# Performance work log

Hardware: AMD Instinct MI355X
Metric: run time of the kernel (lower is better)

Reference implementation:

```python
import jax, jax.numpy as jnp
import numpy as np

WIN = (4, 8, 8)          # window_size (wd, wh, ww)
NUM_HEADS = 8
NW = 64                  # number of distinct shift-mask windows


def _relative_position_index(win):
    wd, wh, ww = win
    coords = np.stack(np.meshgrid(np.arange(wd), np.arange(wh), np.arange(ww), indexing='ij'))
    flat = coords.reshape(3, -1)                       # (3, N)
    rel = flat[:, :, None] - flat[:, None, :]          # (3, N, N)
    rel = rel.transpose(1, 2, 0).astype(np.int64)      # (N, N, 3)
    rel[..., 0] += wd - 1
    rel[..., 1] += wh - 1
    rel[..., 2] += ww - 1
    rel[..., 0] *= (2 * wh - 1) * (2 * ww - 1)
    rel[..., 1] *= (2 * ww - 1)
    return rel.sum(-1)                                 # (N, N)


def setup_inputs() -> dict:
    key = jax.random.key(0)
    ks = jax.random.split(key, 8)
    B_, C = 192, 256
    N = WIN[0] * WIN[1] * WIN[2]                       # 256 tokens per window
    table = (2 * WIN[0] - 1) * (2 * WIN[1] - 1) * (2 * WIN[2] - 1)  # 1575
    s = 0.02
    return {
        'x': jax.random.normal(ks[0], (B_, N, C), jnp.float32),
        'mask': jax.random.normal(ks[1], (NW, N, N), jnp.float32),
        'qkv_w': jax.random.normal(ks[2], (3 * C, C), jnp.float32) * s,
        'qkv_b': jax.random.normal(ks[3], (3 * C,), jnp.float32) * s,
        'proj_w': jax.random.normal(ks[4], (C, C), jnp.float32) * s,
        'proj_b': jax.random.normal(ks[5], (C,), jnp.float32) * s,
        'rel_pos_table': jax.random.normal(ks[6], (table, NUM_HEADS), jnp.float32) * s,
        'rel_pos_index': jnp.asarray(_relative_position_index(WIN), jnp.int32),
    }


def reference(x, mask, qkv_w, qkv_b, proj_w, proj_b, rel_pos_table, rel_pos_index):
    B_, N, C = x.shape
    H = NUM_HEADS
    hd = C // H
    scale = hd ** -0.5
    # qkv projection -> (3, B_, H, N, hd)
    qkv = (x @ qkv_w.T + qkv_b).reshape(B_, N, 3, H, hd).transpose(2, 0, 3, 1, 4)
    q, k, v = qkv[0], qkv[1], qkv[2]
    attn = jnp.einsum('bhnd,bhmd->bhnm', q * scale, k)            # (B_, H, N, N)
    # gathered relative-position bias: (N, N, H) -> (H, N, N)
    bias = rel_pos_table[rel_pos_index.reshape(-1)].reshape(N, N, H).transpose(2, 0, 1)
    attn = attn + bias[None]
    nW = mask.shape[0]
    attn = attn.reshape(B_ // nW, nW, H, N, N) + mask[None, :, None]
    attn = jax.nn.softmax(attn.reshape(B_, H, N, N), axis=-1)
    out = jnp.einsum('bhnm,bhmd->bhnd', attn, v)                  # (B_, H, N, hd)
    out = out.transpose(0, 2, 1, 3).reshape(B_, N, C)
    return out @ proj_w.T + proj_b
```

## Files before the change

kernel.cpp:

```cpp
#include <hip/hip_runtime.h>

typedef unsigned short ushort_t;
typedef __bf16 bf16x8 __attribute__((ext_vector_type(8)));
typedef float floatx4 __attribute__((ext_vector_type(4)));
typedef float floatx16 __attribute__((ext_vector_type(16)));

#define B_WIN 192
#define NTOK 256
#define CDIM 256
#define NHEAD 8
#define HDIM 32
#define NWIN 64
#define MROWS (B_WIN * NTOK)
#define LOG2E 1.4426950408889634f

__device__ __forceinline__ float bf2f(unsigned int b) {
  unsigned int u = (b & 0xffffu) << 16;
  float f; __builtin_memcpy(&f, &u, 4); return f;
}
__device__ __forceinline__ float uasf(unsigned int u) {
  float f; __builtin_memcpy(&f, &u, 4); return f;
}
__device__ __forceinline__ ushort_t f2bf(float f) {
  unsigned int u; __builtin_memcpy(&u, &f, 4);
  u = (u + 0x7fffu + ((u >> 16) & 1u)) >> 16;
  return (ushort_t)u;
}
__device__ __forceinline__ bf16x8 ldg8(const ushort_t* p) {
  return *reinterpret_cast<const bf16x8*>(p);
}
__device__ __forceinline__ void async_copy16(const void* g, void* l) {
  __builtin_amdgcn_global_load_lds(
      (const __attribute__((address_space(1))) unsigned int*)g,
      (__attribute__((address_space(3))) unsigned int*)l, 16, 0, 0);
}
__device__ __forceinline__ float fexp2(float x) {
  return __builtin_amdgcn_exp2f(x);
}
__device__ __forceinline__ unsigned pkbf(float a, float b) {
  return (unsigned)f2bf(a) | ((unsigned)f2bf(b) << 16);
}
__device__ __forceinline__ void plswap(unsigned& a, unsigned& b) {
  auto r = __builtin_amdgcn_permlane32_swap(a, b, false, false);
  a = r[0]; b = r[1];
}

__global__ __launch_bounds__(256) void cvt_f32_bf16(const float* __restrict__ src,
                                                    ushort_t* __restrict__ dst, int n8) {
  int t = blockIdx.x * 256 + threadIdx.x;
  if (t >= n8) return;
  const float4* s = reinterpret_cast<const float4*>(src) + (size_t)t * 2;
  float4 v0 = s[0], v1 = s[1];
  union { ushort_t u[8]; uint4 v; } pk;
  pk.u[0] = f2bf(v0.x); pk.u[1] = f2bf(v0.y); pk.u[2] = f2bf(v0.z); pk.u[3] = f2bf(v0.w);
  pk.u[4] = f2bf(v1.x); pk.u[5] = f2bf(v1.y); pk.u[6] = f2bf(v1.z); pk.u[7] = f2bf(v1.w);
  reinterpret_cast<uint4*>(dst)[t] = pk.v;
}

__global__ __launch_bounds__(256) void cvt_tile_w(const float* __restrict__ src,
                                                  ushort_t* __restrict__ dst, int n) {
  int t = blockIdx.x * 256 + threadIdx.x;
  if (t >= n) return;
  int col = t >> 5;
  int kk = (t & 31) * 8;
  const float4* s = reinterpret_cast<const float4*>(src + (size_t)col * 256 + kk);
  float4 v0 = s[0], v1 = s[1];
  union { ushort_t u[8]; uint4 v; } pk;
  pk.u[0] = f2bf(v0.x); pk.u[1] = f2bf(v0.y); pk.u[2] = f2bf(v0.z); pk.u[3] = f2bf(v0.w);
  pk.u[4] = f2bf(v1.x); pk.u[5] = f2bf(v1.y); pk.u[6] = f2bf(v1.z); pk.u[7] = f2bf(v1.w);
  size_t base = (size_t)(((col >> 4) * 8 + (kk >> 5)) * 512 + ((kk >> 3) & 3) * 128 + (col & 15) * 8);
  *reinterpret_cast<uint4*>(dst + base) = pk.v;
}

__global__ __launch_bounds__(256) void bm_prep(const int* __restrict__ idx,
                                               const float* __restrict__ table,
                                               const float* __restrict__ mask,
                                               ushort_t* __restrict__ bm) {
  const int win = blockIdx.x;
  const int qt = blockIdx.y;
  const int kb = blockIdx.z;
  const int l = threadIdx.x & 63;
  const int rg = threadIdx.x >> 6;
  const int tq = qt * 32 + (l & 31);
  const int hl = l >> 5;
  const int tk0 = kb * 32 + rg * 8 + hl * 4;

  const int4 ids = *reinterpret_cast<const int4*>(idx + tq * 256 + tk0);
  const float4 mv = *reinterpret_cast<const float4*>(mask + (size_t)win * 65536 + tq * 256 + tk0);
  const int idarr[4] = {ids.x, ids.y, ids.z, ids.w};
  const float marr[4] = {mv.x, mv.y, mv.z, mv.w};

  float v[8][4];
  #pragma unroll
  for (int r2 = 0; r2 < 4; ++r2) {
    const float* tr = table + (size_t)idarr[r2] * 8;
    float4 t0 = *reinterpret_cast<const float4*>(tr);
    float4 t1 = *reinterpret_cast<const float4*>(tr + 4);
    float m = marr[r2];
    v[0][r2] = (t0.x + m) * LOG2E; v[1][r2] = (t0.y + m) * LOG2E;
    v[2][r2] = (t0.z + m) * LOG2E; v[3][r2] = (t0.w + m) * LOG2E;
    v[4][r2] = (t1.x + m) * LOG2E; v[5][r2] = (t1.y + m) * LOG2E;
    v[6][r2] = (t1.z + m) * LOG2E; v[7][r2] = (t1.w + m) * LOG2E;
  }
  size_t base = ((size_t)((qt * 8 + kb) * 2 + (rg >> 1))) * 512 + l * 8 + (rg & 1) * 4;
  #pragma unroll
  for (int h = 0; h < 8; ++h) {
    union { ushort_t u[4]; uint2 w; } pk;
    pk.u[0] = f2bf(v[h][0]); pk.u[1] = f2bf(v[h][1]);
    pk.u[2] = f2bf(v[h][2]); pk.u[3] = f2bf(v[h][3]);
    *reinterpret_cast<uint2*>(bm + (((size_t)(win * 8 + h)) << 16) + base) = pk.w;
  }
}

__global__ __launch_bounds__(256) void qkv_gemm(
    const ushort_t* __restrict__ x, const ushort_t* __restrict__ wt,
    const float* __restrict__ qkvb, ushort_t* __restrict__ qws,
    ushort_t* __restrict__ kws, ushort_t* __restrict__ vtws) {
  const int lane = threadIdx.x & 63;
  const int wv = threadIdx.x >> 6;
  const int ln = lane & 15, qd = lane >> 4;
  const int row0 = blockIdx.x * 128 + (wv >> 1) * 64;
  const int col0 = blockIdx.y * 128;
  const int colw = col0 + (wv & 1) * 64;

  floatx4 acc[4][4];
  #pragma unroll
  for (int rt = 0; rt < 4; ++rt)
    #pragma unroll
    for (int ct = 0; ct < 4; ++ct)
      acc[rt][ct] = floatx4{0.f, 0.f, 0.f, 0.f};

  const ushort_t* ap = x + (size_t)(row0 + ln) * 256 + qd * 8;
  const ushort_t* bp = wt + (size_t)col0 * 256 + (wv & 1) * 16384 + qd * 128 + ln * 8;
  bf16x8 abuf[2][4], bbuf[2][4];
  #pragma unroll
  for (int t = 0; t < 4; ++t) {
    abuf[0][t] = ldg8(ap + t * 16 * 256);
    abuf[1][t] = ldg8(ap + t * 16 * 256 + 32);
    bbuf[0][t] = ldg8(bp + (t * 8 + 0) * 512);
    bbuf[1][t] = ldg8(bp + (t * 8 + 1) * 512);
  }

  #pragma unroll
  for (int kt = 0; kt < 8; ++kt) {
    #pragma unroll
    for (int rt = 0; rt < 4; ++rt)
      #pragma unroll
      for (int ct = 0; ct < 4; ++ct)
        acc[rt][ct] = __builtin_amdgcn_mfma_f32_16x16x32_bf16(abuf[kt & 1][rt], bbuf[kt & 1][ct],
                                                              acc[rt][ct], 0, 0, 0);
    if (kt < 6) {
      #pragma unroll
      for (int t = 0; t < 4; ++t) {
        abuf[kt & 1][t] = ldg8(ap + t * 16 * 256 + (kt + 2) * 32);
        bbuf[kt & 1][t] = ldg8(bp + (t * 8 + kt + 2) * 512);
      }
    }
  }

  const int s = colw >> 8;
  const float SCLQ = 0.17677669529663687f * LOG2E;
  #pragma unroll
  for (int ct = 0; ct < 4; ++ct) {
    int colg = colw + ct * 16 + ln;
    float bcol = qkvb[colg];
    int cs = colg & 255;
    int h = cs >> 5, d = cs & 31;
    int dslice = d >> 4, hh = (d >> 3) & 1, j = d & 7;
    #pragma unroll
    for (int rt = 0; rt < 4; ++rt) {
      int rbase = row0 + rt * 16 + qd * 4;
      int bwin = rbase >> 8, tok0 = rbase & 255;
      size_t slab = (size_t)(bwin * 8 + h) * 8192;
      if (s == 2) {
        int kt2 = tok0 >> 4, h2 = (tok0 >> 3) & 1, jj = tok0 & 7;
        union { ushort_t u[4]; uint2 v; } pk;
        #pragma unroll
        for (int i = 0; i < 4; ++i) pk.u[i] = f2bf(acc[rt][ct][i] + bcol);
        *reinterpret_cast<uint2*>(vtws + slab + kt2 * 512 + h2 * 256 + d * 8 + jj) = pk.v;
      } else {
        int blk = tok0 >> 5, c0 = tok0 & 31;
        size_t base = slab + (size_t)((blk * 2 + dslice) * 512 + hh * 256 + c0 * 8 + j);
        if (s == 0) {
          #pragma unroll
          for (int i = 0; i < 4; ++i)
            qws[base + i * 8] = f2bf((acc[rt][ct][i] + bcol) * SCLQ);
        } else {
          #pragma unroll
          for (int i = 0; i < 4; ++i)
            kws[base + i * 8] = f2bf(acc[rt][ct][i] + bcol);
        }
      }
    }
  }
}

__global__ __launch_bounds__(512, 4) void attn_kernel(
    const ushort_t* __restrict__ qws, const ushort_t* __restrict__ kws,
    const ushort_t* __restrict__ vtws, const ushort_t* __restrict__ bm,
    ushort_t* __restrict__ aows) {
  __shared__ __align__(16) ushort_t lds_kv[16384];
  __shared__ float inv_lds[256];
  const int lane = threadIdx.x & 63;
  const int wv = threadIdx.x >> 6;
  const int t = blockIdx.x;
  const int batch = t % 3;
  const int wh = t / 3;
  const int win = wh >> 3, h = wh & 7;
  const int bwin = batch * 64 + win;
  const int bh = bwin * 8 + h;

  {
    const char* kg = (const char*)(kws + (size_t)bh * 8192);
    const char* vg = (const char*)(vtws + (size_t)bh * 8192);
    #pragma unroll
    for (int r = 0; r < 2; ++r) {
      int off = r * 8192 + wv * 1024;
      async_copy16(kg + off + lane * 16, (char*)lds_kv + off);
      async_copy16(vg + off + lane * 16, (char*)lds_kv + 16384 + off);
    }
  }
  __syncthreads();

  const int qt = wv;
  const int hl = lane >> 5;
  const ushort_t* qb = qws + (size_t)bh * 8192 + qt * 1024 + lane * 8;
  const bf16x8 qf0 = ldg8(qb);
  const bf16x8 qf1 = ldg8(qb + 512);
  const ushort_t* bmp = bm + (((size_t)(win * 8 + h)) << 16) + qt * 8192 + lane * 8;

  floatx16 o;
  #pragma unroll
  for (int i = 0; i < 16; ++i) o[i] = 0.f;
  float ss0 = 0.f, ss1 = 0.f, ss2 = 0.f, ss3 = 0.f;

  #pragma unroll
  for (int kb = 0; kb < 8; ++kb) {
    const uint4 b0 = *reinterpret_cast<const uint4*>(bmp + kb * 1024);
    const uint4 b1 = *reinterpret_cast<const uint4*>(bmp + kb * 1024 + 512);
    floatx16 st;
    st[0]  = uasf(b0.x << 16); st[1]  = uasf(b0.x & 0xffff0000u);
    st[2]  = uasf(b0.y << 16); st[3]  = uasf(b0.y & 0xffff0000u);
    st[4]  = uasf(b0.z << 16); st[5]  = uasf(b0.z & 0xffff0000u);
    st[6]  = uasf(b0.w << 16); st[7]  = uasf(b0.w & 0xffff0000u);
    st[8]  = uasf(b1.x << 16); st[9]  = uasf(b1.x & 0xffff0000u);
    st[10] = uasf(b1.y << 16); st[11] = uasf(b1.y & 0xffff0000u);
    st[12] = uasf(b1.z << 16); st[13] = uasf(b1.z & 0xffff0000u);
    st[14] = uasf(b1.w << 16); st[15] = uasf(b1.w & 0xffff0000u);

    const bf16x8 kf0 = *reinterpret_cast<const bf16x8*>(&lds_kv[(kb * 2 + 0) * 512 + lane * 8]);
    const bf16x8 kf1 = *reinterpret_cast<const bf16x8*>(&lds_kv[(kb * 2 + 1) * 512 + lane * 8]);
    st = __builtin_amdgcn_mfma_f32_32x32x16_bf16(kf0, qf0, st, 0, 0, 0);
    st = __builtin_amdgcn_mfma_f32_32x32x16_bf16(kf1, qf1, st, 0, 0, 0);

    #pragma unroll
    for (int i = 0; i < 16; i += 4) {
      float e0 = fexp2(st[i]);     st[i]     = e0; ss0 += e0;
      float e1 = fexp2(st[i + 1]); st[i + 1] = e1; ss1 += e1;
      float e2 = fexp2(st[i + 2]); st[i + 2] = e2; ss2 += e2;
      float e3 = fexp2(st[i + 3]); st[i + 3] = e3; ss3 += e3;
    }

    unsigned p0 = pkbf(st[0], st[1]),   p1 = pkbf(st[2], st[3]);
    unsigned p2 = pkbf(st[4], st[5]),   p3 = pkbf(st[6], st[7]);
    unsigned p4 = pkbf(st[8], st[9]),   p5 = pkbf(st[10], st[11]);
    unsigned p6 = pkbf(st[12], st[13]), p7 = pkbf(st[14], st[15]);
    plswap(p0, p2);
    plswap(p1, p3);
    plswap(p4, p6);
    plswap(p5, p7);
    union { unsigned u[4]; bf16x8 v; } afe, afo;
    afe.u[0] = p0; afe.u[1] = p1; afe.u[2] = p2; afe.u[3] = p3;
    afo.u[0] = p4; afo.u[1] = p5; afo.u[2] = p6; afo.u[3] = p7;

    const bf16x8 bv0 = *reinterpret_cast<const bf16x8*>(&lds_kv[8192 + (kb * 2 + 0) * 512 + lane * 8]);
    const bf16x8 bv1 = *reinterpret_cast<const bf16x8*>(&lds_kv[8192 + (kb * 2 + 1) * 512 + lane * 8]);
    o = __builtin_amdgcn_mfma_f32_32x32x16_bf16(afe.v, bv0, o, 0, 0, 0);
    o = __builtin_amdgcn_mfma_f32_32x32x16_bf16(afo.v, bv1, o, 0, 0, 0);
  }

  float ssum = (ss0 + ss1) + (ss2 + ss3);
  ssum += __shfl_xor(ssum, 32, 64);
  const float inv = 1.0f / ssum;
  inv_lds[wv * 32 + (lane & 31)] = inv;
  __builtin_amdgcn_s_waitcnt(0);
  const float4 iv0 = *reinterpret_cast<const float4*>(&inv_lds[wv * 32 + 0 + hl * 4]);
  const float4 iv1 = *reinterpret_cast<const float4*>(&inv_lds[wv * 32 + 8 + hl * 4]);
  const float4 iv2 = *reinterpret_cast<const float4*>(&inv_lds[wv * 32 + 16 + hl * 4]);
  const float4 iv3 = *reinterpret_cast<const float4*>(&inv_lds[wv * 32 + 24 + hl * 4]);

  const int d = lane & 31;
  ushort_t* op = aows + (((size_t)bwin * 256 + qt * 32 + 4 * hl) << 8) + h * 32 + d;
  op[0 * 256]  = f2bf(o[0]  * iv0.x); op[1 * 256]  = f2bf(o[1]  * iv0.y);
  op[2 * 256]  = f2bf(o[2]  * iv0.z); op[3 * 256]  = f2bf(o[3]  * iv0.w);
  op[8 * 256]  = f2bf(o[4]  * iv1.x); op[9 * 256]  = f2bf(o[5]  * iv1.y);
  op[10 * 256] = f2bf(o[6]  * iv1.z); op[11 * 256] = f2bf(o[7]  * iv1.w);
  op[16 * 256] = f2bf(o[8]  * iv2.x); op[17 * 256] = f2bf(o[9]  * iv2.y);
  op[18 * 256] = f2bf(o[10] * iv2.z); op[19 * 256] = f2bf(o[11] * iv2.w);
  op[24 * 256] = f2bf(o[12] * iv3.x); op[25 * 256] = f2bf(o[13] * iv3.y);
  op[26 * 256] = f2bf(o[14] * iv3.z); op[27 * 256] = f2bf(o[15] * iv3.w);
}

__global__ __launch_bounds__(256) void proj_gemm(
    const ushort_t* __restrict__ a_, const ushort_t* __restrict__ wt,
    const float* __restrict__ pb, float* __restrict__ out) {
  const int lane = threadIdx.x & 63;
  const int wv = threadIdx.x >> 6;
  const int ln = lane & 15, qd = lane >> 4;
  const int row0 = blockIdx.x * 128 + (wv >> 1) * 64;
  const int col0 = blockIdx.y * 128;
  const int colw = col0 + (wv & 1) * 64;

  floatx4 acc[4][4];
  #pragma unroll
  for (int rt = 0; rt < 4; ++rt)
    #pragma unroll
    for (int ct = 0; ct < 4; ++ct)
      acc[rt][ct] = floatx4{0.f, 0.f, 0.f, 0.f};

  const ushort_t* ap = a_ + (size_t)(row0 + ln) * 256 + qd * 8;
  const ushort_t* bp = wt + (size_t)col0 * 256 + (wv & 1) * 16384 + qd * 128 + ln * 8;
  bf16x8 abuf[2][4], bbuf[2][4];
  #pragma unroll
  for (int t = 0; t < 4; ++t) {
    abuf[0][t] = ldg8(ap + t * 16 * 256);
    abuf[1][t] = ldg8(ap + t * 16 * 256 + 32);
    bbuf[0][t] = ldg8(bp + (t * 8 + 0) * 512);
    bbuf[1][t] = ldg8(bp + (t * 8 + 1) * 512);
  }

  #pragma unroll
  for (int kt = 0; kt < 8; ++kt) {
    #pragma unroll
    for (int rt = 0; rt < 4; ++rt)
      #pragma unroll
      for (int ct = 0; ct < 4; ++ct)
        acc[rt][ct] = __builtin_amdgcn_mfma_f32_16x16x32_bf16(abuf[kt & 1][rt], bbuf[kt & 1][ct],
                                                              acc[rt][ct], 0, 0, 0);
    if (kt < 6) {
      #pragma unroll
      for (int t = 0; t < 4; ++t) {
        abuf[kt & 1][t] = ldg8(ap + t * 16 * 256 + (kt + 2) * 32);
        bbuf[kt & 1][t] = ldg8(bp + (t * 8 + kt + 2) * 512);
      }
    }
  }

  #pragma unroll
  for (int ct = 0; ct < 4; ++ct) {
    int colg = colw + ct * 16 + ln;
    float bcol = pb[colg];
    #pragma unroll
    for (int rt = 0; rt < 4; ++rt) {
      int rbase = row0 + rt * 16 + qd * 4;
      #pragma unroll
      for (int i = 0; i < 4; ++i)
        out[(size_t)(rbase + i) * 256 + colg] = acc[rt][ct][i] + bcol;
    }
  }
}

extern "C" void kernel_launch(void* const* d_in, const int* in_sizes, int n_in,
                              void* d_out, int out_size, void* d_ws, size_t ws_size,
                              hipStream_t stream) {
  const float* x      = (const float*)d_in[0];
  const float* mask   = (const float*)d_in[1];
  const float* qkv_w  = (const float*)d_in[2];
  const float* qkv_b  = (const float*)d_in[3];
  const float* proj_w = (const float*)d_in[4];
  const float* proj_b = (const float*)d_in[5];
  const float* table  = (const float*)d_in[6];
  const int*   idx    = (const int*)d_in[7];
  float* out = (float*)d_out;

  char* ws = (char*)d_ws;
  const size_t SZ = (size_t)MROWS * CDIM * 2;
  ushort_t* xbf  = (ushort_t*)(ws);
  ushort_t* qws  = (ushort_t*)(ws + SZ);
  ushort_t* kws  = (ushort_t*)(ws + 2 * SZ);
  ushort_t* vtws = (ushort_t*)(ws + 3 * SZ);
  ushort_t* aows = (ushort_t*)(ws + 4 * SZ);
  ushort_t* bmws = (ushort_t*)(ws + 5 * SZ);
  ushort_t* wqkvbf  = (ushort_t*)(ws + 5 * SZ + 67108864);
  ushort_t* wprojbf = (ushort_t*)(ws + 5 * SZ + 67108864 + 393216);

  cvt_f32_bf16<<<dim3(6144), dim3(256), 0, stream>>>(x, xbf, 12582912 / 8);
  cvt_tile_w<<<dim3(96), dim3(256), 0, stream>>>(qkv_w, wqkvbf, 768 * 32);
  cvt_tile_w<<<dim3(32), dim3(256), 0, stream>>>(proj_w, wprojbf, 256 * 32);
  bm_prep<<<dim3(64, 8, 8), dim3(256), 0, stream>>>(idx, table, mask, bmws);
  qkv_gemm<<<dim3(384, 6), dim3(256), 0, stream>>>(xbf, wqkvbf, qkv_b, qws, kws, vtws);
  attn_kernel<<<dim3(1536), dim3(512), 0, stream>>>(qws, kws, vtws, bmws, aows);
  proj_gemm<<<dim3(384, 2), dim3(256), 0, stream>>>(aows, wprojbf, proj_b, out);
}
```

Measured before the change: 283.9 us.

## Split combined bias+mask into separate per-window mask and per-head bias buffers

Instead of precomputing a 64x8 window-by-head combined bias+mask tensor in bf16, this stores the mask per window and the relative-position bias per head, and adds them inside the attention kernel. That shrinks the prep output and the attention kernel's streamed footprint, and the small bias buffer stays cache-resident. In exchange, each score element needs an extra load and an add, and summing two rounded bf16 values adds a little error. The GEMM grids are also flattened with an XCD-aware block remap so that each XCD works on a contiguous range of row tiles, which should improve L2 reuse.

New measurement: 272.2 us. -4.1%, faster.

```diff
diff --git a/kernel.cpp b/kernel.cpp
--- a/kernel.cpp
+++ b/kernel.cpp
@@ -14,10 +14,6 @@
 #define MROWS (B_WIN * NTOK)
 #define LOG2E 1.4426950408889634f
 
-__device__ __forceinline__ float bf2f(unsigned int b) {
-  unsigned int u = (b & 0xffffu) << 16;
-  float f; __builtin_memcpy(&f, &u, 4); return f;
-}
 __device__ __forceinline__ float uasf(unsigned int u) {
   float f; __builtin_memcpy(&f, &u, 4); return f;
 }
@@ -72,10 +68,8 @@
   *reinterpret_cast<uint4*>(dst + base) = pk.v;
 }
 
-__global__ __launch_bounds__(256) void bm_prep(const int* __restrict__ idx,
-                                               const float* __restrict__ table,
-                                               const float* __restrict__ mask,
-                                               ushort_t* __restrict__ bm) {
+__global__ __launch_bounds__(256) void mask_prep(const float* __restrict__ mask,
+                                                 ushort_t* __restrict__ mf) {
   const int win = blockIdx.x;
   const int qt = blockIdx.y;
   const int kb = blockIdx.z;
@@ -84,23 +78,36 @@
   const int tq = qt * 32 + (l & 31);
   const int hl = l >> 5;
   const int tk0 = kb * 32 + rg * 8 + hl * 4;
-
+  const float4 mv = *reinterpret_cast<const float4*>(mask + (size_t)win * 65536 + tq * 256 + tk0);
+  union { ushort_t u[4]; uint2 w; } pk;
+  pk.u[0] = f2bf(mv.x * LOG2E); pk.u[1] = f2bf(mv.y * LOG2E);
+  pk.u[2] = f2bf(mv.z * LOG2E); pk.u[3] = f2bf(mv.w * LOG2E);
+  size_t base = ((size_t)((qt * 8 + kb) * 2 + (rg >> 1))) * 512 + l * 8 + (rg & 1) * 4;
+  *reinterpret_cast<uint2*>(mf + ((size_t)win << 16) + base) = pk.w;
+}
+
+__global__ __launch_bounds__(256) void bias_prep(const int* __restrict__ idx,
+                                                 const float* __restrict__ table,
+                                                 ushort_t* __restrict__ bf) {
+  const int qt = blockIdx.x;
+  const int kb = blockIdx.y;
+  const int l = threadIdx.x & 63;
+  const int rg = threadIdx.x >> 6;
+  const int tq = qt * 32 + (l & 31);
+  const int hl = l >> 5;
+  const int tk0 = kb * 32 + rg * 8 + hl * 4;
   const int4 ids = *reinterpret_cast<const int4*>(idx + tq * 256 + tk0);
-  const float4 mv = *reinterpret_cast<const float4*>(mask + (size_t)win * 65536 + tq * 256 + tk0);
   const int idarr[4] = {ids.x, ids.y, ids.z, ids.w};
-  const float marr[4] = {mv.x, mv.y, mv.z, mv.w};
-
   float v[8][4];
   #pragma unroll
   for (int r2 = 0; r2 < 4; ++r2) {
     const float* tr = table + (size_t)idarr[r2] * 8;
     float4 t0 = *reinterpret_cast<const float4*>(tr);
     float4 t1 = *reinterpret_cast<const float4*>(tr + 4);
-    float m = marr[r2];
-    v[0][r2] = (t0.x + m) * LOG2E; v[1][r2] = (t0.y + m) * LOG2E;
-    v[2][r2] = (t0.z + m) * LOG2E; v[3][r2] = (t0.w + m) * LOG2E;
-    v[4][r2] = (t1.x + m) * LOG2E; v[5][r2] = (t1.y + m) * LOG2E;
-    v[6][r2] = (t1.z + m) * LOG2E; v[7][r2] = (t1.w + m) * LOG2E;
+    v[0][r2] = t0.x * LOG2E; v[1][r2] = t0.y * LOG2E;
+    v[2][r2] = t0.z * LOG2E; v[3][r2] = t0.w * LOG2E;
+    v[4][r2] = t1.x * LOG2E; v[5][r2] = t1.y * LOG2E;
+    v[6][r2] = t1.z * LOG2E; v[7][r2] = t1.w * LOG2E;
   }
   size_t base = ((size_t)((qt * 8 + kb) * 2 + (rg >> 1))) * 512 + l * 8 + (rg & 1) * 4;
   #pragma unroll
@@ -108,7 +115,7 @@
     union { ushort_t u[4]; uint2 w; } pk;
     pk.u[0] = f2bf(v[h][0]); pk.u[1] = f2bf(v[h][1]);
     pk.u[2] = f2bf(v[h][2]); pk.u[3] = f2bf(v[h][3]);
-    *reinterpret_cast<uint2*>(bm + (((size_t)(win * 8 + h)) << 16) + base) = pk.w;
+    *reinterpret_cast<uint2*>(bf + ((size_t)h << 16) + base) = pk.w;
   }
 }
 
@@ -119,8 +126,12 @@
   const int lane = threadIdx.x & 63;
   const int wv = threadIdx.x >> 6;
   const int ln = lane & 15, qd = lane >> 4;
-  const int row0 = blockIdx.x * 128 + (wv >> 1) * 64;
-  const int col0 = blockIdx.y * 128;
+  const int b = blockIdx.x;
+  const int xcd = b & 7, lb = b >> 3;
+  const int rtile = xcd * 48 + (lb % 48);
+  const int ctile = lb / 48;
+  const int row0 = rtile * 128 + (wv >> 1) * 64;
+  const int col0 = ctile * 128;
   const int colw = col0 + (wv & 1) * 64;
 
   floatx4 acc[4][4];
@@ -197,8 +208,8 @@
 
 __global__ __launch_bounds__(512, 4) void attn_kernel(
     const ushort_t* __restrict__ qws, const ushort_t* __restrict__ kws,
-    const ushort_t* __restrict__ vtws, const ushort_t* __restrict__ bm,
-    ushort_t* __restrict__ aows) {
+    const ushort_t* __restrict__ vtws, const ushort_t* __restrict__ mf,
+    const ushort_t* __restrict__ bfr, ushort_t* __restrict__ aows) {
   __shared__ __align__(16) ushort_t lds_kv[16384];
   __shared__ float inv_lds[256];
   const int lane = threadIdx.x & 63;
@@ -227,7 +238,8 @@
   const ushort_t* qb = qws + (size_t)bh * 8192 + qt * 1024 + lane * 8;
   const bf16x8 qf0 = ldg8(qb);
   const bf16x8 qf1 = ldg8(qb + 512);
-  const ushort_t* bmp = bm + (((size_t)(win * 8 + h)) << 16) + qt * 8192 + lane * 8;
+  const ushort_t* mp = mf + ((size_t)win << 16) + qt * 8192 + lane * 8;
+  const ushort_t* cp = bfr + ((size_t)h << 16) + qt * 8192 + lane * 8;
 
   floatx16 o;
   #pragma unroll
@@ -236,17 +248,27 @@
 
   #pragma unroll
   for (int kb = 0; kb < 8; ++kb) {
-    const uint4 b0 = *reinterpret_cast<const uint4*>(bmp + kb * 1024);
-    const uint4 b1 = *reinterpret_cast<const uint4*>(bmp + kb * 1024 + 512);
+    const uint4 m0 = *reinterpret_cast<const uint4*>(mp + kb * 1024);
+    const uint4 m1 = *reinterpret_cast<const uint4*>(mp + kb * 1024 + 512);
+    const uint4 c0 = *reinterpret_cast<const uint4*>(cp + kb * 1024);
+    const uint4 c1 = *reinterpret_cast<const uint4*>(cp + kb * 1024 + 512);
     floatx16 st;
-    st[0]  = uasf(b0.x << 16); st[1]  = uasf(b0.x & 0xffff0000u);
-    st[2]  = uasf(b0.y << 16); st[3]  = uasf(b0.y & 0xffff0000u);
-    st[4]  = uasf(b0.z << 16); st[5]  = uasf(b0.z & 0xffff0000u);
-    st[6]  = uasf(b0.w << 16); st[7]  = uasf(b0.w & 0xffff0000u);
-    st[8]  = uasf(b1.x << 16); st[9]  = uasf(b1.x & 0xffff0000u);
-    st[10] = uasf(b1.y << 16); st[11] = uasf(b1.y & 0xffff0000u);
-    st[12] = uasf(b1.z << 16); st[13] = uasf(b1.z & 0xffff0000u);
-    st[14] = uasf(b1.w << 16); st[15] = uasf(b1.w & 0xffff0000u);
+    st[0]  = uasf(m0.x << 16) + uasf(c0.x << 16);
+    st[1]  = uasf(m0.x & 0xffff0000u) + uasf(c0.x & 0xffff0000u);
+    st[2]  = uasf(m0.y << 16) + uasf(c0.y << 16);
+    st[3]  = uasf(m0.y & 0xffff0000u) + uasf(c0.y & 0xffff0000u);
+    st[4]  = uasf(m0.z << 16) + uasf(c0.z << 16);
+    st[5]  = uasf(m0.z & 0xffff0000u) + uasf(c0.z & 0xffff0000u);
+    st[6]  = uasf(m0.w << 16) + uasf(c0.w << 16);
+    st[7]  = uasf(m0.w & 0xffff0000u) + uasf(c0.w & 0xffff0000u);
+    st[8]  = uasf(m1.x << 16) + uasf(c1.x << 16);
+    st[9]  = uasf(m1.x & 0xffff0000u) + uasf(c1.x & 0xffff0000u);
+    st[10] = uasf(m1.y << 16) + uasf(c1.y << 16);
+    st[11] = uasf(m1.y & 0xffff0000u) + uasf(c1.y & 0xffff0000u);
+    st[12] = uasf(m1.z << 16) + uasf(c1.z << 16);
+    st[13] = uasf(m1.z & 0xffff0000u) + uasf(c1.z & 0xffff0000u);
+    st[14] = uasf(m1.w << 16) + uasf(c1.w << 16);
+    st[15] = uasf(m1.w & 0xffff0000u) + uasf(c1.w & 0xffff0000u);
 
     const bf16x8 kf0 = *reinterpret_cast<const bf16x8*>(&lds_kv[(kb * 2 + 0) * 512 + lane * 8]);
     const bf16x8 kf1 = *reinterpret_cast<const bf16x8*>(&lds_kv[(kb * 2 + 1) * 512 + lane * 8]);
@@ -307,8 +329,12 @@
   const int lane = threadIdx.x & 63;
   const int wv = threadIdx.x >> 6;
   const int ln = lane & 15, qd = lane >> 4;
-  const int row0 = blockIdx.x * 128 + (wv >> 1) * 64;
-  const int col0 = blockIdx.y * 128;
+  const int b = blockIdx.x;
+  const int xcd = b & 7, lb = b >> 3;
+  const int rtile = xcd * 48 + (lb % 48);
+  const int ctile = lb / 48;
+  const int row0 = rtile * 128 + (wv >> 1) * 64;
+  const int col0 = ctile * 128;
   const int colw = col0 + (wv & 1) * 64;
 
   floatx4 acc[4][4];
@@ -380,15 +406,17 @@
   ushort_t* kws  = (ushort_t*)(ws + 2 * SZ);
   ushort_t* vtws = (ushort_t*)(ws + 3 * SZ);
   ushort_t* aows = (ushort_t*)(ws + 4 * SZ);
-  ushort_t* bmws = (ushort_t*)(ws + 5 * SZ);
-  ushort_t* wqkvbf  = (ushort_t*)(ws + 5 * SZ + 67108864);
-  ushort_t* wprojbf = (ushort_t*)(ws + 5 * SZ + 67108864 + 393216);
+  ushort_t* mfws = (ushort_t*)(ws + 5 * SZ);
+  ushort_t* bfws = (ushort_t*)(ws + 5 * SZ + 8388608);
+  ushort_t* wqkvbf  = (ushort_t*)(ws + 5 * SZ + 8388608 + 1048576);
+  ushort_t* wprojbf = (ushort_t*)(ws + 5 * SZ + 8388608 + 1048576 + 393216);
 
   cvt_f32_bf16<<<dim3(6144), dim3(256), 0, stream>>>(x, xbf, 12582912 / 8);
   cvt_tile_w<<<dim3(96), dim3(256), 0, stream>>>(qkv_w, wqkvbf, 768 * 32);
   cvt_tile_w<<<dim3(32), dim3(256), 0, stream>>>(proj_w, wprojbf, 256 * 32);
-  bm_prep<<<dim3(64, 8, 8), dim3(256), 0, stream>>>(idx, table, mask, bmws);
-  qkv_gemm<<<dim3(384, 6), dim3(256), 0, stream>>>(xbf, wqkvbf, qkv_b, qws, kws, vtws);
-  attn_kernel<<<dim3(1536), dim3(512), 0, stream>>>(qws, kws, vtws, bmws, aows);
-  proj_gemm<<<dim3(384, 2), dim3(256), 0, stream>>>(aows, wprojbf, proj_b, out);
-}
+  mask_prep<<<dim3(64, 8, 8), dim3(256), 0, stream>>>(mask, mfws);
+  bias_prep<<<dim3(8, 8), dim3(256), 0, stream>>>(idx, table, bfws);
+  qkv_gemm<<<dim3(2304), dim3(256), 0, stream>>>(xbf, wqkvbf, qkv_b, qws, kws, vtws);
+  attn_kernel<<<dim3(1536), dim3(512), 0, stream>>>(qws, kws, vtws, mfws, bfws, aows);
+  proj_gemm<<<dim3(768), dim3(256), 0, stream>>>(aows, wprojbf, proj_b, out);
+}
```
